# Optimization experiments

Hardware: AMD Instinct MI355X
Metric: run time of the kernel (lower is better)

Reference implementation:

```python
import jax, jax.numpy as jnp
import numpy as np

B, T, W, R, N = 32, 256, 128, 4, 128
IFACE = R * W + 3 * W + 5 * R + 3   # 919
INSZ = (R + 1) * W                  # 640
DELTA = 1e-6

def _lstm_step(x, h, c, Wih, Whh, bih, bhh):
    g = x @ Wih.T + bih + h @ Whh.T + bhh
    i, f, gg, o = jnp.split(g, 4, axis=-1)
    c = jax.nn.sigmoid(f) * c + jax.nn.sigmoid(i) * jnp.tanh(gg)
    return jax.nn.sigmoid(o) * jnp.tanh(c), c

def _cosine(mem, keys):
    # mem [b,n,w], keys [b,h,w] -> [b,h,n]
    mn = mem / (jnp.linalg.norm(mem, axis=2, keepdims=True) + DELTA)
    kn = keys / (jnp.linalg.norm(keys, axis=2, keepdims=True) + DELTA)
    return jnp.einsum('bhw,bnw->bhn', kn, mn)

def _memory_step(xi, st):
    # xi: [b, IFACE] interface vector; st: DNC memory state
    mem, link, prec, rw, ww, usage = st
    b = xi.shape[0]
    o1 = R * W; o2 = o1 + R; o3 = o2 + W; o4 = o3 + 1
    o5 = o4 + W; o6 = o5 + W; o7 = o6 + R; o8 = o7 + 1; o9 = o8 + 1
    read_keys = jnp.tanh(xi[:, :o1].reshape(b, R, W))
    read_str = jax.nn.softplus(xi[:, o1:o2])
    write_key = jnp.tanh(xi[:, o2:o3])
    write_str = jax.nn.softplus(xi[:, o3:o4])
    erase = jax.nn.sigmoid(xi[:, o4:o5])
    write_vec = jnp.tanh(xi[:, o5:o6])
    free_gates = jax.nn.sigmoid(xi[:, o6:o7])
    alloc_gate = jax.nn.sigmoid(xi[:, o7:o8])
    write_gate = jax.nn.sigmoid(xi[:, o8:o9])
    read_modes = jax.nn.softmax(xi[:, o9:].reshape(b, R, 3), axis=-1)
    # usage vector update (single write head)
    usage = usage + (1 - usage) * ww
    usage = usage * jnp.prod(1 - free_gates[:, :, None] * rw, axis=1)
    # write content weighting [b,n]
    wc = jax.nn.softmax(_cosine(mem, write_key[:, None, :])[:, 0, :] * write_str, axis=1)
    # allocation weighting: sort ascending, exclusive cumprod, unsort
    u = DELTA + (1 - DELTA) * usage
    phi = jnp.argsort(u, axis=1)
    su = jnp.take_along_axis(u, phi, axis=1)
    prod_su = jnp.cumprod(jnp.concatenate([jnp.ones((b, 1), u.dtype), su], axis=1), axis=1)[:, :-1]
    alloc = jnp.take_along_axis((1 - su) * prod_su, jnp.argsort(phi, axis=1), axis=1)
    # write weighting [b,n]
    ww = write_gate * (alloc_gate * alloc + (1 - alloc_gate) * wc)
    # erase then write
    mem = mem * (1 - ww[:, :, None] * erase[:, None, :]) + ww[:, :, None] * write_vec[:, None, :]
    # temporal link matrix [b,n,n], zero diagonal
    link = (1 - ww[:, :, None] - ww[:, None, :]) * link + ww[:, :, None] * prec[:, None, :]
    link = link * (1 - jnp.eye(N, dtype=link.dtype))
    prec = (1 - jnp.sum(ww, axis=1, keepdims=True)) * prec + ww
    # read weighting: content + forward/backward temporal modes
    rc = jax.nn.softmax(_cosine(mem, read_keys) * read_str[:, :, None], axis=2)
    fw = jnp.einsum('bij,brj->bri', link, rw)
    bw = jnp.einsum('brj,bji->bri', rw, link)
    rw = read_modes[:, :, 0:1] * bw + read_modes[:, :, 1:2] * fw + read_modes[:, :, 2:3] * rc
    read_vecs = jnp.einsum('brn,bnw->bwr', rw, mem)  # [b,w,r] as used by controller
    return read_vecs, (mem, link, prec, rw, ww, usage)

def _forward(input, enc_Wih, enc_Whh, enc_bih, enc_bhh, ctl_Wih, ctl_Whh, ctl_bih, ctl_bhh, iface_W, iface_b, out_W, out_b):
    dt = input.dtype
    h0 = jnp.zeros((B, W), dt)
    def enc_step(carry, x_t):
        h, c = _lstm_step(x_t, carry[0], carry[1], enc_Wih, enc_Whh, enc_bih, enc_bhh)
        return (h, c), h
    _, enc = jax.lax.scan(enc_step, (h0, h0), jnp.swapaxes(input, 0, 1))  # enc: [T,B,W]
    z = lambda *s: jnp.zeros(s, dt)
    mem0 = (z(B, N, W), z(B, N, N), z(B, N), z(B, R, N), z(B, N), z(B, N))
    def step(carry, enc_t):
        h, c, rv, mst = carry
        # cat([b,w,1],[b,w,r]) then flatten -> interleaved per memory-cell element, as in torch
        x = jnp.concatenate([enc_t[:, :, None], rv], axis=2).reshape(B, INSZ)
        h, c = _lstm_step(x, h, c, ctl_Wih, ctl_Whh, ctl_bih, ctl_bhh)
        xi = h @ iface_W.T + iface_b
        rv, mst = _memory_step(xi, mst)
        out_t = jnp.concatenate([h, rv.reshape(B, W * R)], axis=1) @ out_W.T + out_b
        return (h, c, rv, mst), out_t
    _, outs = jax.lax.scan(step, (h0, h0, z(B, W, R), mem0), enc)
    return jnp.swapaxes(outs, 0, 1)  # [B,T,W]

def setup_inputs():
    key = jax.random.key(0)
    ks = jax.random.split(key, 8)
    p = lambda k, s: jax.random.normal(k, s, jnp.float32) * 0.05
    return {
        'input': jax.random.normal(ks[0], (B, T, W), jnp.float32),
        'source_lengths': jnp.full((B,), T, jnp.int32),
        'enc_Wih': p(ks[1], (4 * W, W)), 'enc_Whh': p(ks[2], (4 * W, W)),
        'enc_bih': jnp.zeros((4 * W,), jnp.float32), 'enc_bhh': jnp.zeros((4 * W,), jnp.float32),
        'ctl_Wih': p(ks[3], (4 * W, INSZ)), 'ctl_Whh': p(ks[4], (4 * W, W)),
        'ctl_bih': jnp.zeros((4 * W,), jnp.float32), 'ctl_bhh': jnp.zeros((4 * W,), jnp.float32),
        'iface_W': p(ks[5], (IFACE, W)), 'iface_b': jnp.zeros((IFACE,), jnp.float32),
        'out_W': p(ks[6], (W, INSZ)), 'out_b': jnp.zeros((W,), jnp.float32),
    }

def reference(input, source_lengths, enc_Wih, enc_Whh, enc_bih, enc_bhh, ctl_Wih, ctl_Whh, ctl_bih, ctl_bhh, iface_W, iface_b, out_W, out_b):
    # source_lengths are all == T (full-length sequences), so pack/pad is identity.
    return _forward(input, enc_Wih, enc_Whh, enc_bih, enc_bhh, ctl_Wih, ctl_Whh, ctl_bih, ctl_bhh, iface_W, iface_b, out_W, out_b)
```

## Files before the change

kernel.cpp:

```cpp
#include <hip/hip_runtime.h>

typedef unsigned short u16;
typedef unsigned int u32;

#define NT 1024
#define Bv 32
#define Tv 256
#define Wv 128
#define Rv 4
#define Nv 128
#define DELTAv 1e-6f

__device__ __forceinline__ float bf2f(u16 u){
  union { u32 i; float f; } c; c.i = ((u32)u) << 16; return c.f;
}
__device__ __forceinline__ u16 f2bf(float f){
  union { float f; u32 u; } c; c.f = f;
  u32 u = c.u;
  return (u16)((u + 0x7fffu + ((u >> 16) & 1u)) >> 16);
}
__device__ __forceinline__ void unp(u32 v, float& a, float& b){
  union { u32 i; float f; } c0, c1;
  c0.i = v << 16; c1.i = v & 0xffff0000u;
  a = c0.f; b = c1.f;
}
__device__ __forceinline__ float sigm(float x){ return 1.0f / (1.0f + __expf(-x)); }
__device__ __forceinline__ float softplusf(float x){ return fmaxf(x, 0.f) + log1pf(__expf(-fabsf(x))); }
__device__ __forceinline__ float wredsum(float v){
  #pragma unroll
  for (int o = 32; o > 0; o >>= 1) v += __shfl_down(v, o, 64);
  return v;
}
__device__ __forceinline__ float wredmax(float v){
  #pragma unroll
  for (int o = 32; o > 0; o >>= 1) v = fmaxf(v, __shfl_down(v, o, 64));
  return v;
}
__device__ __forceinline__ float ldval(const void* p, int idx, int dt32){
  return dt32 ? ((const float*)p)[idx] : bf2f(((const u16*)p)[idx]);
}

template<int ITERS, int STRIDE>
__device__ __forceinline__ float gemv_bf(const u32* __restrict__ wp, const float* __restrict__ xp){
  float a0 = 0.f, a1 = 0.f;
  u32 wb[8];
  #pragma unroll
  for (int i = 0; i < 8; i++) wb[i] = wp[i * STRIDE];
  #pragma unroll 1
  for (int c = 0; c < ITERS - 8; c += 8){
    u32 wn[8];
    #pragma unroll
    for (int i = 0; i < 8; i++) wn[i] = wp[(c + 8 + i) * STRIDE];
    #pragma unroll
    for (int i = 0; i < 8; i++){
      float w0, w1; unp(wb[i], w0, w1);
      float2 x2 = *(const float2*)(xp + 2 * (c + i));
      a0 = fmaf(x2.x, w0, a0); a1 = fmaf(x2.y, w1, a1);
      wb[i] = wn[i];
    }
  }
  #pragma unroll
  for (int i = 0; i < 8; i++){
    float w0, w1; unp(wb[i], w0, w1);
    float2 x2 = *(const float2*)(xp + 2 * (ITERS - 8 + i));
    a0 = fmaf(x2.x, w0, a0); a1 = fmaf(x2.y, w1, a1);
  }
  return a0 + a1;
}

__global__ void detect_dtype(const u16* __restrict__ buf, int* __restrict__ flag){
  int lane = threadIdx.x;
  float crazy = 0.f;
  for (int i = 0; i < 4; i++){
    u16 v = buf[lane * 4 + i];
    int e = (v >> 7) & 0xFF;
    if (e != 0 && (e < 117 || e > 137)) crazy += 1.f;
  }
  crazy = wredsum(crazy);
  if (lane == 0) flag[0] = (crazy >= 32.f) ? 1 : 0;
}

__device__ __forceinline__ u16 rdbf(const void* s, size_t idx, int f32){
  return f32 ? f2bf(((const float*)s)[idx]) : ((const u16*)s)[idx];
}

__global__ void pack_w(const void* __restrict__ src, u32* __restrict__ dst,
                       int Js, int Jd, int K, const int* __restrict__ flag){
  int j = blockIdx.x * 256 + threadIdx.x;
  int k2 = blockIdx.y;
  if (j >= Jd) return;
  u16 lo = 0, hi = 0;
  if (j < Js){
    lo = rdbf(src, (size_t)j * K + 2 * k2, flag[0]);
    hi = rdbf(src, (size_t)j * K + 2 * k2 + 1, flag[0]);
  }
  dst[(size_t)k2 * Jd + j] = (u32)lo | ((u32)hi << 16);
}

__device__ __forceinline__ int permctl(int c){
  if (c < 128) return 5 * c;
  int q = c - 128; return 5 * (q & 127) + 1 + (q >> 7);
}
__device__ __forceinline__ int permout(int c){
  if (c < 128) return c;
  int q = c - 128; return 128 + 4 * (q & 127) + (q >> 7);
}

__global__ void pack_ctl(const void* __restrict__ src, u32* __restrict__ dst,
                         const int* __restrict__ flag){
  int j = blockIdx.x * 256 + threadIdx.x;
  int k2 = blockIdx.y;
  if (j >= 512) return;
  u16 lo = rdbf(src, (size_t)j * 640 + permctl(2 * k2), flag[0]);
  u16 hi = rdbf(src, (size_t)j * 640 + permctl(2 * k2 + 1), flag[0]);
  dst[(size_t)k2 * 512 + j] = (u32)lo | ((u32)hi << 16);
}

__global__ void pack_out(const void* __restrict__ src, u32* __restrict__ dst,
                         const int* __restrict__ flag){
  int j = threadIdx.x;
  int k2 = blockIdx.y;
  if (j >= 128) return;
  u16 lo = rdbf(src, (size_t)j * 640 + permout(2 * k2), flag[0]);
  u16 hi = rdbf(src, (size_t)j * 640 + permout(2 * k2 + 1), flag[0]);
  dst[(size_t)k2 * 128 + j] = (u32)lo | ((u32)hi << 16);
}

__global__ void fill_half(u16* __restrict__ p, int n){
  int i = blockIdx.x * 256 + threadIdx.x;
  if (i < n) p[i] = 0x3F00;
}

__global__ __launch_bounds__(NT) void dnc_main(
    const void* __restrict__ input,
    const void* __restrict__ enc_bih_g, const void* __restrict__ enc_bhh_g,
    const void* __restrict__ ctl_bih_g, const void* __restrict__ ctl_bhh_g,
    const void* __restrict__ iface_b_g, const void* __restrict__ out_b_g,
    const u32* __restrict__ encPW, const u32* __restrict__ ctlPW,
    const u32* __restrict__ ifPW, const u32* __restrict__ outPW,
    void* __restrict__ outp, const int* __restrict__ dtflag)
{
  const int bid = blockIdx.x;
  const int tid = threadIdx.x;
  const int lane = tid & 63;
  const int wid = tid >> 6;
  const int dt32 = dtflag[0];

  __shared__ __align__(16) float memS[Nv * 129];
  __shared__ __align__(16) float linkS[Nv * 129];
  __shared__ __align__(16) float pp[NT];
  __shared__ __align__(16) float ppE[NT];
  __shared__ __align__(16) float xhC[768];
  __shared__ __align__(16) float xinS[128];
  __shared__ __align__(16) float rkeyS[512], rwS[512], rcS[512];
  __shared__ __align__(16) float wkeyS[128], eraseS[128], wvecS[128];
  __shared__ __align__(16) float wwS[128], usageS[128], precS[128], wcS[128];
  __shared__ __align__(16) float uS[128], sortedU[128], scanA[128], alS[128], sqS[128];
  __shared__ __align__(16) float encBias[512], ctlBias[512];
  __shared__ __align__(16) float outBias[128];
  __shared__ float rstrS[4], fgS[4], rmRaw[12], rmS[12], scal[8];

  const int wE = (tid >= 919) ? (tid - 919) : (tid < 23 ? 105 + tid : -1);
  float cE = 0.f;
  float cC = 0.f;

  if (tid < 512){
    encBias[tid] = ldval(enc_bih_g, tid, dt32) + ldval(enc_bhh_g, tid, dt32);
    ctlBias[tid] = ldval(ctl_bih_g, tid, dt32) + ldval(ctl_bhh_g, tid, dt32);
    rwS[tid] = 0.f;
  }
  if (tid < 768) xhC[tid] = 0.f;
  if (tid < 128){
    outBias[tid] = ldval(out_b_g, tid, dt32);
    wwS[tid] = 0.f; usageS[tid] = 0.f; precS[tid] = 0.f;
  }
  for (int i = tid; i < Nv * 129; i += NT){ memS[i] = 0.f; linkS[i] = 0.f; }
  if (tid < 64){
    int idx = (bid * Tv + 0) * Wv + 2 * tid;
    xinS[2 * tid] = ldval(input, idx, dt32);
    xinS[2 * tid + 1] = ldval(input, idx + 1, dt32);
  }
  __syncthreads();

  if (tid >= 512){
    int o = tid - 512;
    ppE[o] = gemv_bf<64, 512>(encPW + o, xinS);
  }
  __syncthreads();
  if (wE >= 0){
    float g0 = ppE[wE] + encBias[wE];
    float g1 = ppE[128 + wE] + encBias[128 + wE];
    float g2 = ppE[256 + wE] + encBias[256 + wE];
    float g3 = ppE[384 + wE] + encBias[384 + wE];
    float cn = sigm(g1) * cE + sigm(g0) * tanhf(g2);
    cE = cn;
    xhC[wE] = sigm(g3) * tanhf(cn);
  }
  if (tid >= 64 && tid < 128){
    int w2 = (tid - 64) * 2;
    int idx = (bid * Tv + 1) * Wv + w2;
    xinS[w2] = ldval(input, idx, dt32);
    xinS[w2 + 1] = ldval(input, idx + 1, dt32);
  }
  __syncthreads();

  for (int t = 0; t < Tv; ++t){
    if (t > 0 && tid < 128){
      float o = outBias[tid];
      #pragma unroll
      for (int s = 0; s < 8; s++) o += ppE[s * 128 + tid];
      size_t oi = ((size_t)bid * Tv + (t - 1)) * Wv + tid;
      if (dt32) ((float*)outp)[oi] = o;
      else ((u16*)outp)[oi] = f2bf(o);
    }
    {
      int s = tid >> 9, o = tid & 511;
      pp[tid] = gemv_bf<192, 512>(ctlPW + (s * 192) * 512 + o, xhC + s * 384);
    }
    __syncthreads();

    if (tid < 128){
      float g0 = pp[tid] + pp[512 + tid] + ctlBias[tid];
      float g1 = pp[128 + tid] + pp[640 + tid] + ctlBias[128 + tid];
      float g2 = pp[256 + tid] + pp[768 + tid] + ctlBias[256 + tid];
      float g3 = pp[384 + tid] + pp[896 + tid] + ctlBias[384 + tid];
      float cn = sigm(g1) * cC + sigm(g0) * tanhf(g2);
      cC = cn;
      xhC[640 + tid] = sigm(g3) * tanhf(cn);
    } else if (tid >= 512){
      int o = tid - 512;
      ppE[o] = gemv_bf<64, 512>(encPW + o, xinS)
             + gemv_bf<64, 512>(encPW + 64 * 512 + o, xhC);
    }
    __syncthreads();

    if (tid < 919){
      pp[tid] = ldval(iface_b_g, tid, dt32) + gemv_bf<64, 928>(ifPW + tid, xhC + 640);
    }
    if (wE >= 0){
      float g0 = ppE[wE] + encBias[wE];
      float g1 = ppE[128 + wE] + encBias[128 + wE];
      float g2 = ppE[256 + wE] + encBias[256 + wE];
      float g3 = ppE[384 + wE] + encBias[384 + wE];
      float cn = sigm(g1) * cE + sigm(g0) * tanhf(g2);
      cE = cn;
      xhC[wE] = sigm(g3) * tanhf(cn);
    }
    __syncthreads();

    if (tid < 919){
      float v = pp[tid];
      if (tid < 512) rkeyS[tid] = tanhf(v);
      else if (tid < 516) rstrS[tid - 512] = softplusf(v);
      else if (tid < 644) wkeyS[tid - 516] = tanhf(v);
      else if (tid == 644) scal[0] = softplusf(v);
      else if (tid < 773) eraseS[tid - 645] = sigm(v);
      else if (tid < 901) wvecS[tid - 773] = tanhf(v);
      else if (tid < 905) fgS[tid - 901] = sigm(v);
      else if (tid == 905) scal[1] = sigm(v);
      else if (tid == 906) scal[2] = sigm(v);
      else rmRaw[tid - 907] = v;
    } else if (tid >= 928 && tid < 992){
      int w2 = (tid - 928) * 2;
      int col = (t + 2 < Tv) ? t + 2 : Tv - 1;
      int idx = (bid * Tv + col) * Wv + w2;
      xinS[w2] = ldval(input, idx, dt32);
      xinS[w2 + 1] = ldval(input, idx + 1, dt32);
    }
    __syncthreads();

    if (wid < 5){
      float* arr = (wid < 4) ? (rkeyS + wid * 128) : wkeyS;
      float a = arr[lane], bq = arr[lane + 64];
      float s = wredsum(a * a + bq * bq);
      s = __shfl(s, 0, 64);
      float inv = 1.0f / (sqrtf(s) + DELTAv);
      arr[lane] = a * inv; arr[lane + 64] = bq * inv;
    } else if (wid < 7){
      int n = (wid - 5) * 64 + lane;
      float us = usageS[n];
      us = us + (1.f - us) * wwS[n];
      float ret = (1.f - fgS[0] * rwS[n]) * (1.f - fgS[1] * rwS[128 + n]) *
                  (1.f - fgS[2] * rwS[256 + n]) * (1.f - fgS[3] * rwS[384 + n]);
      us *= ret;
      usageS[n] = us;
      uS[n] = DELTAv + (1.f - DELTAv) * us;
    } else if (tid >= 448 && tid < 452){
      int r = tid - 448;
      float m0 = rmRaw[3 * r], m1 = rmRaw[3 * r + 1], m2 = rmRaw[3 * r + 2];
      float mx = fmaxf(m0, fmaxf(m1, m2));
      float e0 = __expf(m0 - mx), e1 = __expf(m1 - mx), e2 = __expf(m2 - mx);
      float s = e0 + e1 + e2;
      rmS[3 * r] = e0 / s; rmS[3 * r + 1] = e1 / s; rmS[3 * r + 2] = e2 / s;
    } else if (wid >= 8 && wid < 10){
      int n = (wid - 8) * 64 + lane;
      float sq = 0.f;
      #pragma unroll 8
      for (int j = 0; j < 128; j++){
        float m = memS[n * 129 + j];
        sq = fmaf(m, m, sq);
      }
      sqS[n] = sq;
    }
    __syncthreads();

    if (tid < 128){
      float dt = 0.f;
      #pragma unroll 8
      for (int j = 0; j < 128; j++) dt = fmaf(memS[tid * 129 + j], wkeyS[j], dt);
      wcS[tid] = dt / (sqrtf(sqS[tid]) + DELTAv) * scal[0];
    }
    __syncthreads();

    if (wid == 0){
      float a = wcS[lane], bq = wcS[lane + 64];
      float mx = wredmax(fmaxf(a, bq)); mx = __shfl(mx, 0, 64);
      float ea = __expf(a - mx), eb = __expf(bq - mx);
      float s = wredsum(ea + eb); s = __shfl(s, 0, 64);
      wcS[lane] = ea / s; wcS[lane + 64] = eb / s;
    } else if (wid == 1){
      int l = lane;
      float u0 = uS[l], u1 = uS[64 + l];
      int r0 = 0, r1 = 0;
      for (int m = 0; m < 128; m++){
        float um = uS[m];
        r0 += (um < u0) || (um == u0 && m < l);
        r1 += (um < u1) || (um == u1 && m < 64 + l);
      }
      sortedU[r0] = u0; sortedU[r1] = u1;
      float a = sortedU[2 * l], bq = sortedU[2 * l + 1];
      float p = a * bq;
      float incl = p;
      #pragma unroll
      for (int o = 1; o < 64; o <<= 1){
        float tv = __shfl_up(incl, o, 64);
        if (l >= o) incl *= tv;
      }
      float exh = __shfl_up(incl, 1, 64);
      if (l == 0) exh = 1.f;
      scanA[2 * l] = exh;
      scanA[2 * l + 1] = exh * a;
      float ex0 = scanA[r0], ex1 = scanA[r1];
      alS[l] = (1.f - u0) * ex0;
      alS[64 + l] = (1.f - u1) * ex1;
    }
    __syncthreads();

    if (wid == 0){
      float w0v = scal[2] * (scal[1] * alS[lane] + (1.f - scal[1]) * wcS[lane]);
      float w1v = scal[2] * (scal[1] * alS[64 + lane] + (1.f - scal[1]) * wcS[64 + lane]);
      wwS[lane] = w0v; wwS[64 + lane] = w1v;
      float s = wredsum(w0v + w1v);
      if (lane == 0) scal[3] = s;
    }
    __syncthreads();

    #pragma unroll
    for (int it = 0; it < 16; it++){
      int e = it * NT + tid;
      int n = e >> 7, w = e & 127;
      float wwn = wwS[n];
      float m = memS[n * 129 + w];
      memS[n * 129 + w] = m * (1.f - wwn * eraseS[w]) + wwn * wvecS[w];
      float l = linkS[n * 129 + w];
      linkS[n * 129 + w] = (n == w) ? 0.f
        : ((1.f - wwn - wwS[w]) * l + wwn * precS[w]);
    }
    __syncthreads();

    if (tid < 128){
      float sq = 0.f, d0 = 0.f, d1 = 0.f, d2 = 0.f, d3 = 0.f;
      #pragma unroll 4
      for (int j = 0; j < 128; j++){
        float m = memS[tid * 129 + j];
        sq = fmaf(m, m, sq);
        d0 = fmaf(m, rkeyS[j], d0);
        d1 = fmaf(m, rkeyS[128 + j], d1);
        d2 = fmaf(m, rkeyS[256 + j], d2);
        d3 = fmaf(m, rkeyS[384 + j], d3);
      }
      float inv = 1.f / (sqrtf(sq) + DELTAv);
      rcS[tid]       = d0 * inv * rstrS[0];
      rcS[128 + tid] = d1 * inv * rstrS[1];
      rcS[256 + tid] = d2 * inv * rstrS[2];
      rcS[384 + tid] = d3 * inv * rstrS[3];
    } else if (tid < 256){
      int n = tid - 128;
      precS[n] = (1.f - scal[3]) * precS[n] + wwS[n];
    } else if (tid < 768){
      int o = tid - 256, r = o >> 7, i = o & 127;
      const float* rwp = rwS + r * 128;
      float acc = 0.f;
      #pragma unroll 8
      for (int j = 0; j < 128; j++) acc = fmaf(rwp[j], linkS[i * 129 + j], acc);
      pp[o] = acc;
    } else {
      int o2 = tid - 768, i = o2 & 127;
      int r1 = o2 >> 7, r2 = r1 + 2;
      const float* rw1 = rwS + r1 * 128;
      const float* rw2 = rwS + r2 * 128;
      float accA = 0.f, accB = 0.f;
      #pragma unroll 8
      for (int j = 0; j < 128; j++){
        float l = linkS[j * 129 + i];
        accA = fmaf(rw1[j], l, accA);
        accB = fmaf(rw2[j], l, accB);
      }
      pp[512 + o2] = accA;
      pp[512 + o2 + 256] = accB;
    }
    __syncthreads();

    if (wid < 4){
      int r = wid;
      float a = rcS[r * 128 + lane], bq = rcS[r * 128 + 64 + lane];
      float mx = wredmax(fmaxf(a, bq)); mx = __shfl(mx, 0, 64);
      float ea = __expf(a - mx), eb = __expf(bq - mx);
      float s = wredsum(ea + eb); s = __shfl(s, 0, 64);
      float pa = ea / s, pb = eb / s;
      int o0 = r * 128 + lane, o1 = o0 + 64;
      rwS[o0] = rmS[3 * r] * pp[512 + o0] + rmS[3 * r + 1] * pp[o0] + rmS[3 * r + 2] * pa;
      rwS[o1] = rmS[3 * r] * pp[512 + o1] + rmS[3 * r + 1] * pp[o1] + rmS[3 * r + 2] * pb;
    }
    __syncthreads();

    if (tid < 512){
      int r = tid >> 7, w = tid & 127;
      const float* rwp = rwS + r * 128;
      float acc = 0.f;
      #pragma unroll 8
      for (int n = 0; n < 128; n++) acc = fmaf(rwp[n], memS[n * 129 + w], acc);
      xhC[128 + tid] = acc;
    } else {
      int s = (tid - 512) >> 7, j = tid & 127;
      ppE[tid] = gemv_bf<16, 128>(outPW + (s * 16) * 128 + j, xhC + 640 + 32 * s);
    }
    __syncthreads();

    if (tid < 512){
      int s = tid >> 7, j = tid & 127;
      ppE[tid] = gemv_bf<64, 128>(outPW + (64 + s * 64) * 128 + j, xhC + 128 + 128 * s);
    }
    __syncthreads();
  }

  if (tid < 128){
    float o = outBias[tid];
    #pragma unroll
    for (int s = 0; s < 8; s++) o += ppE[s * 128 + tid];
    size_t oi = ((size_t)bid * Tv + (Tv - 1)) * Wv + tid;
    if (dt32) ((float*)outp)[oi] = o;
    else ((u16*)outp)[oi] = f2bf(o);
  }
}

extern "C" void kernel_launch(void* const* d_in, const int* in_sizes, int n_in,
                              void* d_out, int out_size, void* d_ws, size_t ws_size,
                              hipStream_t stream) {
  (void)in_sizes; (void)n_in;
  const void* input   = d_in[0];
  const void* enc_Wih = d_in[2];
  const void* enc_Whh = d_in[3];
  const void* enc_bih = d_in[4];
  const void* enc_bhh = d_in[5];
  const void* ctl_Wih = d_in[6];
  const void* ctl_Whh = d_in[7];
  const void* ctl_bih = d_in[8];
  const void* ctl_bhh = d_in[9];
  const void* iface_W = d_in[10];
  const void* iface_b = d_in[11];
  const void* out_W   = d_in[12];
  const void* out_b   = d_in[13];

  char* ws = (char*)d_ws;
  size_t off = 0;
  int* dtflag = (int*)(ws + off); off += 256;
  u32* encPW = (u32*)(ws + off); off += (size_t)128 * 512 * 4;
  u32* ctlPW = (u32*)(ws + off); off += (size_t)384 * 512 * 4;
  u32* ifPW  = (u32*)(ws + off); off += (size_t)64 * 928 * 4;
  u32* outPW = (u32*)(ws + off); off += (size_t)320 * 128 * 4;
  const size_t need_bytes = off;

  if (ws_size < need_bytes){
    fill_half<<<dim3((out_size + 255) / 256), dim3(256), 0, stream>>>((u16*)d_out, out_size);
    return;
  }

  detect_dtype<<<dim3(1), dim3(64), 0, stream>>>((const u16*)input, dtflag);

  pack_w<<<dim3(2, 64), 256, 0, stream>>>(enc_Wih, encPW, 512, 512, 128, dtflag);
  pack_w<<<dim3(2, 64), 256, 0, stream>>>(enc_Whh, encPW + 64 * 512, 512, 512, 128, dtflag);
  pack_ctl<<<dim3(2, 320), 256, 0, stream>>>(ctl_Wih, ctlPW, dtflag);
  pack_w<<<dim3(2, 64), 256, 0, stream>>>(ctl_Whh, ctlPW + 320 * 512, 512, 512, 128, dtflag);
  pack_w<<<dim3(4, 64), 256, 0, stream>>>(iface_W, ifPW, 919, 928, 128, dtflag);
  pack_out<<<dim3(1, 320), 128, 0, stream>>>(out_W, outPW, dtflag);

  dnc_main<<<dim3(Bv), dim3(NT), 0, stream>>>(
      input, enc_bih, enc_bhh, ctl_bih, ctl_bhh, iface_b, out_b,
      encPW, ctlPW, ifPW, outPW, d_out, dtflag);
}
```

Before: 10.67 ms.

## Register-block gemvs, use readlane broadcasts, and remap thread roles per phase

Each thread now computes two output columns in the LSTM and interface gemvs, so input-vector loads from LDS are shared across both columns. The memory and link matrix-vector products are reorganised so fewer threads each compute several read heads, with the per-element weights broadcast through v_readlane instead of LDS reads. The encoder input is double-buffered and prefetched, and the thread roles are reassigned so the encoder gemv overlaps the controller gemv. The cost is fewer active threads per phase and more serial work per thread, which can lengthen the critical path.

```diff
diff --git a/kernel.cpp b/kernel.cpp
--- a/kernel.cpp
+++ b/kernel.cpp
@@ -38,6 +38,11 @@
 }
 __device__ __forceinline__ float ldval(const void* p, int idx, int dt32){
   return dt32 ? ((const float*)p)[idx] : bf2f(((const u16*)p)[idx]);
+}
+__device__ __forceinline__ float rl(float v, int l){
+  union { int i; float f; } c;
+  c.i = __builtin_amdgcn_readlane(__float_as_int(v), l);
+  return c.f;
 }
 
 template<int ITERS, int STRIDE>
@@ -68,6 +73,41 @@
   return a0 + a1;
 }
 
+template<int ITERS, int STRIDE>
+__device__ __forceinline__ void gemv2_bf(const u32* __restrict__ wp0, const u32* __restrict__ wp1,
+                                         const float* __restrict__ xp, float& r0, float& r1){
+  float a0 = 0.f, a1 = 0.f, b0 = 0.f, b1 = 0.f;
+  u32 wa[4], wb[4];
+  #pragma unroll
+  for (int i = 0; i < 4; i++){ wa[i] = wp0[i * STRIDE]; wb[i] = wp1[i * STRIDE]; }
+  #pragma unroll 1
+  for (int c = 0; c < ITERS - 4; c += 4){
+    u32 na[4], nb[4];
+    #pragma unroll
+    for (int i = 0; i < 4; i++){ na[i] = wp0[(c + 4 + i) * STRIDE]; nb[i] = wp1[(c + 4 + i) * STRIDE]; }
+    #pragma unroll
+    for (int i = 0; i < 4; i++){
+      float2 x2 = *(const float2*)(xp + 2 * (c + i));
+      float w0, w1;
+      unp(wa[i], w0, w1);
+      a0 = fmaf(x2.x, w0, a0); a1 = fmaf(x2.y, w1, a1);
+      unp(wb[i], w0, w1);
+      b0 = fmaf(x2.x, w0, b0); b1 = fmaf(x2.y, w1, b1);
+      wa[i] = na[i]; wb[i] = nb[i];
+    }
+  }
+  #pragma unroll
+  for (int i = 0; i < 4; i++){
+    float2 x2 = *(const float2*)(xp + 2 * (ITERS - 4 + i));
+    float w0, w1;
+    unp(wa[i], w0, w1);
+    a0 = fmaf(x2.x, w0, a0); a1 = fmaf(x2.y, w1, a1);
+    unp(wb[i], w0, w1);
+    b0 = fmaf(x2.x, w0, b0); b1 = fmaf(x2.y, w1, b1);
+  }
+  r0 = a0 + a1; r1 = b0 + b1;
+}
+
 __global__ void detect_dtype(const u16* __restrict__ buf, int* __restrict__ flag){
   int lane = threadIdx.x;
   float crazy = 0.f;
@@ -151,7 +191,7 @@
   __shared__ __align__(16) float pp[NT];
   __shared__ __align__(16) float ppE[NT];
   __shared__ __align__(16) float xhC[768];
-  __shared__ __align__(16) float xinS[128];
+  __shared__ __align__(16) float xin2[2][128];
   __shared__ __align__(16) float rkeyS[512], rwS[512], rcS[512];
   __shared__ __align__(16) float wkeyS[128], eraseS[128], wvecS[128];
   __shared__ __align__(16) float wwS[128], usageS[128], precS[128], wcS[128];
@@ -160,7 +200,6 @@
   __shared__ __align__(16) float outBias[128];
   __shared__ float rstrS[4], fgS[4], rmRaw[12], rmS[12], scal[8];
 
-  const int wE = (tid >= 919) ? (tid - 919) : (tid < 23 ? 105 + tid : -1);
   float cE = 0.f;
   float cC = 0.f;
 
@@ -177,45 +216,64 @@
   for (int i = tid; i < Nv * 129; i += NT){ memS[i] = 0.f; linkS[i] = 0.f; }
   if (tid < 64){
     int idx = (bid * Tv + 0) * Wv + 2 * tid;
-    xinS[2 * tid] = ldval(input, idx, dt32);
-    xinS[2 * tid + 1] = ldval(input, idx + 1, dt32);
+    xin2[0][2 * tid] = ldval(input, idx, dt32);
+    xin2[0][2 * tid + 1] = ldval(input, idx + 1, dt32);
+  } else if (tid >= 64 && tid < 128){
+    int w2 = (tid - 64) * 2;
+    int idx = (bid * Tv + 1) * Wv + w2;
+    xin2[1][w2] = ldval(input, idx, dt32);
+    xin2[1][w2 + 1] = ldval(input, idx + 1, dt32);
   }
   __syncthreads();
 
-  if (tid >= 512){
+  if (tid >= 512 && tid < 768){
     int o = tid - 512;
-    ppE[o] = gemv_bf<64, 512>(encPW + o, xinS);
+    float r0, r1;
+    gemv2_bf<64, 512>(encPW + o, encPW + o + 256, xin2[0], r0, r1);
+    rcS[o] = r0; rcS[o + 256] = r1;
   }
   __syncthreads();
-  if (wE >= 0){
-    float g0 = ppE[wE] + encBias[wE];
-    float g1 = ppE[128 + wE] + encBias[128 + wE];
-    float g2 = ppE[256 + wE] + encBias[256 + wE];
-    float g3 = ppE[384 + wE] + encBias[384 + wE];
+  if (tid >= 896){
+    int w = tid - 896;
+    float g0 = rcS[w] + encBias[w];
+    float g1 = rcS[128 + w] + encBias[128 + w];
+    float g2 = rcS[256 + w] + encBias[256 + w];
+    float g3 = rcS[384 + w] + encBias[384 + w];
     float cn = sigm(g1) * cE + sigm(g0) * tanhf(g2);
     cE = cn;
-    xhC[wE] = sigm(g3) * tanhf(cn);
-  }
-  if (tid >= 64 && tid < 128){
-    int w2 = (tid - 64) * 2;
-    int idx = (bid * Tv + 1) * Wv + w2;
-    xinS[w2] = ldval(input, idx, dt32);
-    xinS[w2 + 1] = ldval(input, idx + 1, dt32);
+    xhC[w] = sigm(g3) * tanhf(cn);
   }
   __syncthreads();
 
   for (int t = 0; t < Tv; ++t){
-    if (t > 0 && tid < 128){
-      float o = outBias[tid];
-      #pragma unroll
-      for (int s = 0; s < 8; s++) o += ppE[s * 128 + tid];
-      size_t oi = ((size_t)bid * Tv + (t - 1)) * Wv + tid;
-      if (dt32) ((float*)outp)[oi] = o;
-      else ((u16*)outp)[oi] = f2bf(o);
-    }
-    {
-      int s = tid >> 9, o = tid & 511;
-      pp[tid] = gemv_bf<192, 512>(ctlPW + (s * 192) * 512 + o, xhC + s * 384);
+    if (tid < 512){
+      int s = tid >> 8, o = tid & 255;
+      float r0, r1;
+      gemv2_bf<192, 512>(ctlPW + (s * 192) * 512 + o, ctlPW + (s * 192) * 512 + o + 256,
+                         xhC + s * 384, r0, r1);
+      pp[s * 512 + o] = r0;
+      pp[s * 512 + o + 256] = r1;
+    } else if (tid < 768){
+      int o = tid - 512;
+      float r0, r1;
+      gemv2_bf<64, 512>(encPW + o, encPW + o + 256, xin2[(t + 1) & 1], r0, r1);
+      rcS[o] = r0; rcS[o + 256] = r1;
+    } else if (tid < 896){
+      if (t > 0){
+        int w = tid - 768;
+        float o = outBias[w];
+        #pragma unroll
+        for (int s = 0; s < 8; s++) o += ppE[s * 128 + w];
+        size_t oi = ((size_t)bid * Tv + (t - 1)) * Wv + w;
+        if (dt32) ((float*)outp)[oi] = o;
+        else ((u16*)outp)[oi] = f2bf(o);
+      }
+    } else if (tid >= 960){
+      int w2 = (tid - 960) * 2;
+      int col = (t + 2 < Tv) ? t + 2 : Tv - 1;
+      int idx = (bid * Tv + col) * Wv + w2;
+      xin2[t & 1][w2] = ldval(input, idx, dt32);
+      xin2[t & 1][w2 + 1] = ldval(input, idx + 1, dt32);
     }
     __syncthreads();
 
@@ -227,24 +285,29 @@
       float cn = sigm(g1) * cC + sigm(g0) * tanhf(g2);
       cC = cn;
       xhC[640 + tid] = sigm(g3) * tanhf(cn);
-    } else if (tid >= 512){
+    } else if (tid >= 512 && tid < 768){
       int o = tid - 512;
-      ppE[o] = gemv_bf<64, 512>(encPW + o, xinS)
-             + gemv_bf<64, 512>(encPW + 64 * 512 + o, xhC);
-    }
-    __syncthreads();
-
-    if (tid < 919){
-      pp[tid] = ldval(iface_b_g, tid, dt32) + gemv_bf<64, 928>(ifPW + tid, xhC + 640);
-    }
-    if (wE >= 0){
-      float g0 = ppE[wE] + encBias[wE];
-      float g1 = ppE[128 + wE] + encBias[128 + wE];
-      float g2 = ppE[256 + wE] + encBias[256 + wE];
-      float g3 = ppE[384 + wE] + encBias[384 + wE];
+      float r0, r1;
+      gemv2_bf<64, 512>(encPW + 64 * 512 + o, encPW + 64 * 512 + o + 256, xhC, r0, r1);
+      ppE[o] = rcS[o] + r0;
+      ppE[o + 256] = rcS[o + 256] + r1;
+    }
+    __syncthreads();
+
+    if (tid < 464){
+      float r0, r1;
+      gemv2_bf<64, 928>(ifPW + tid, ifPW + tid + 464, xhC + 640, r0, r1);
+      pp[tid] = r0 + ldval(iface_b_g, tid, dt32);
+      pp[tid + 464] = r1 + ((tid + 464 < 919) ? ldval(iface_b_g, tid + 464, dt32) : 0.f);
+    } else if (tid >= 896){
+      int w = tid - 896;
+      float g0 = ppE[w] + encBias[w];
+      float g1 = ppE[128 + w] + encBias[128 + w];
+      float g2 = ppE[256 + w] + encBias[256 + w];
+      float g3 = ppE[384 + w] + encBias[384 + w];
       float cn = sigm(g1) * cE + sigm(g0) * tanhf(g2);
       cE = cn;
-      xhC[wE] = sigm(g3) * tanhf(cn);
+      xhC[w] = sigm(g3) * tanhf(cn);
     }
     __syncthreads();
 
@@ -260,12 +323,6 @@
       else if (tid == 905) scal[1] = sigm(v);
       else if (tid == 906) scal[2] = sigm(v);
       else rmRaw[tid - 907] = v;
-    } else if (tid >= 928 && tid < 992){
-      int w2 = (tid - 928) * 2;
-      int col = (t + 2 < Tv) ? t + 2 : Tv - 1;
-      int idx = (bid * Tv + col) * Wv + w2;
-      xinS[w2] = ldval(input, idx, dt32);
-      xinS[w2 + 1] = ldval(input, idx + 1, dt32);
     }
     __syncthreads();
 
@@ -305,9 +362,13 @@
     __syncthreads();
 
     if (tid < 128){
+      float wk0 = wkeyS[lane], wk1 = wkeyS[64 + lane];
       float dt = 0.f;
-      #pragma unroll 8
-      for (int j = 0; j < 128; j++) dt = fmaf(memS[tid * 129 + j], wkeyS[j], dt);
+      #pragma unroll 128
+      for (int j = 0; j < 128; j++){
+        float m = memS[tid * 129 + j];
+        dt = fmaf(rl((j < 64) ? wk0 : wk1, j & 63), m, dt);
+      }
       wcS[tid] = dt / (sqrtf(sqS[tid]) + DELTAv) * scal[0];
     }
     __syncthreads();
@@ -369,45 +430,50 @@
     __syncthreads();
 
     if (tid < 128){
-      float sq = 0.f, d0 = 0.f, d1 = 0.f, d2 = 0.f, d3 = 0.f;
-      #pragma unroll 4
+      int i = tid;
+      float rwreg[8];
+      #pragma unroll
+      for (int q = 0; q < 8; q++) rwreg[q] = rwS[q * 64 + lane];
+      float f0 = 0.f, f1 = 0.f, f2 = 0.f, f3 = 0.f;
+      float b0 = 0.f, b1 = 0.f, b2 = 0.f, b3 = 0.f;
+      #pragma unroll 128
       for (int j = 0; j < 128; j++){
-        float m = memS[tid * 129 + j];
-        sq = fmaf(m, m, sq);
-        d0 = fmaf(m, rkeyS[j], d0);
-        d1 = fmaf(m, rkeyS[128 + j], d1);
-        d2 = fmaf(m, rkeyS[256 + j], d2);
-        d3 = fmaf(m, rkeyS[384 + j], d3);
-      }
-      float inv = 1.f / (sqrtf(sq) + DELTAv);
-      rcS[tid]       = d0 * inv * rstrS[0];
-      rcS[128 + tid] = d1 * inv * rstrS[1];
-      rcS[256 + tid] = d2 * inv * rstrS[2];
-      rcS[384 + tid] = d3 * inv * rstrS[3];
+        float lr = linkS[i * 129 + j];
+        float lc = linkS[j * 129 + i];
+        float w0 = rl(rwreg[j >> 6], j & 63);
+        float w1 = rl(rwreg[2 + (j >> 6)], j & 63);
+        float w2 = rl(rwreg[4 + (j >> 6)], j & 63);
+        float w3 = rl(rwreg[6 + (j >> 6)], j & 63);
+        f0 = fmaf(w0, lr, f0); b0 = fmaf(w0, lc, b0);
+        f1 = fmaf(w1, lr, f1); b1 = fmaf(w1, lc, b1);
+        f2 = fmaf(w2, lr, f2); b2 = fmaf(w2, lc, b2);
+        f3 = fmaf(w3, lr, f3); b3 = fmaf(w3, lc, b3);
+      }
+      pp[i] = f0; pp[128 + i] = f1; pp[256 + i] = f2; pp[384 + i] = f3;
+      pp[512 + i] = b0; pp[640 + i] = b1; pp[768 + i] = b2; pp[896 + i] = b3;
     } else if (tid < 256){
       int n = tid - 128;
+      float kreg[8];
+      #pragma unroll
+      for (int q = 0; q < 8; q++) kreg[q] = rkeyS[q * 64 + lane];
+      float sq = 0.f, d0 = 0.f, d1 = 0.f, d2 = 0.f, d3 = 0.f;
+      #pragma unroll 128
+      for (int j = 0; j < 128; j++){
+        float m = memS[n * 129 + j];
+        sq = fmaf(m, m, sq);
+        d0 = fmaf(rl(kreg[j >> 6], j & 63), m, d0);
+        d1 = fmaf(rl(kreg[2 + (j >> 6)], j & 63), m, d1);
+        d2 = fmaf(rl(kreg[4 + (j >> 6)], j & 63), m, d2);
+        d3 = fmaf(rl(kreg[6 + (j >> 6)], j & 63), m, d3);
+      }
+      float inv = 1.f / (sqrtf(sq) + DELTAv);
+      rcS[n]       = d0 * inv * rstrS[0];
+      rcS[128 + n] = d1 * inv * rstrS[1];
+      rcS[256 + n] = d2 * inv * rstrS[2];
+      rcS[384 + n] = d3 * inv * rstrS[3];
+    } else if (tid < 384){
+      int n = tid - 256;
       precS[n] = (1.f - scal[3]) * precS[n] + wwS[n];
-    } else if (tid < 768){
-      int o = tid - 256, r = o >> 7, i = o & 127;
-      const float* rwp = rwS + r * 128;
-      float acc = 0.f;
-      #pragma unroll 8
-      for (int j = 0; j < 128; j++) acc = fmaf(rwp[j], linkS[i * 129 + j], acc);
-      pp[o] = acc;
-    } else {
-      int o2 = tid - 768, i = o2 & 127;
-      int r1 = o2 >> 7, r2 = r1 + 2;
-      const float* rw1 = rwS + r1 * 128;
-      const float* rw2 = rwS + r2 * 128;
-      float accA = 0.f, accB = 0.f;
-      #pragma unroll 8
-      for (int j = 0; j < 128; j++){
-        float l = linkS[j * 129 + i];
-        accA = fmaf(rw1[j], l, accA);
-        accB = fmaf(rw2[j], l, accB);
-      }
-      pp[512 + o2] = accA;
-      pp[512 + o2 + 256] = accB;
     }
     __syncthreads();
 
@@ -424,14 +490,25 @@
     }
     __syncthreads();
 
-    if (tid < 512){
-      int r = tid >> 7, w = tid & 127;
-      const float* rwp = rwS + r * 128;
-      float acc = 0.f;
-      #pragma unroll 8
-      for (int n = 0; n < 128; n++) acc = fmaf(rwp[n], memS[n * 129 + w], acc);
-      xhC[128 + tid] = acc;
-    } else {
+    if (tid < 128){
+      int w = tid;
+      float rwreg[8];
+      #pragma unroll
+      for (int q = 0; q < 8; q++) rwreg[q] = rwS[q * 64 + lane];
+      float a0 = 0.f, a1 = 0.f, a2 = 0.f, a3 = 0.f;
+      #pragma unroll 128
+      for (int n = 0; n < 128; n++){
+        float m = memS[n * 129 + w];
+        a0 = fmaf(rl(rwreg[n >> 6], n & 63), m, a0);
+        a1 = fmaf(rl(rwreg[2 + (n >> 6)], n & 63), m, a1);
+        a2 = fmaf(rl(rwreg[4 + (n >> 6)], n & 63), m, a2);
+        a3 = fmaf(rl(rwreg[6 + (n >> 6)], n & 63), m, a3);
+      }
+      xhC[128 + w] = a0;
+      xhC[256 + w] = a1;
+      xhC[384 + w] = a2;
+      xhC[512 + w] = a3;
+    } else if (tid >= 512){
       int s = (tid - 512) >> 7, j = tid & 127;
       ppE[tid] = gemv_bf<16, 128>(outPW + (s * 16) * 128 + j, xhC + 640 + 32 * s);
     }
```

Measured after the change: 10.89 ms. 2.1% more time.
